# Kernel tuning notes

Hardware: AMD Instinct MI355X
Metric: run time of the kernel (lower is better)

Reference implementation:

```python
import jax, jax.numpy as jnp
import numpy as np

PATCH = 16
CH = 3


def setup_inputs() -> dict:
    key = jax.random.key(0)
    k1, k2, k3 = jax.random.split(key, 3)
    B, H = 16, 512
    embed_dim = PATCH * PATCH * CH  # 768
    x = jax.random.normal(k1, (B, CH, H, H), dtype=jnp.float32)
    fan_in = CH * PATCH * PATCH
    w = jax.random.normal(k2, (embed_dim, CH, PATCH, PATCH), dtype=jnp.float32) / np.float32(np.sqrt(fan_in))
    b = jax.random.normal(k3, (embed_dim,), dtype=jnp.float32) * 0.01
    return {"x": x, "w": w, "b": b}


def reference(x, w, b):
    p = w.shape[2]                      # patch_size
    B, C, imgsize, _ = x.shape
    pn = imgsize // p                   # patch_num (NOTE: pre-padding count, as in source)
    # zero-pad by one patch on every side
    xp = jnp.pad(x, ((0, 0), (0, 0), (p, p), (p, p)))
    # strided patch-embed conv: [B, embed_dim, pn+2, pn+2]
    xt = jax.lax.conv_general_dilated(xp, w, window_strides=(p, p), padding='VALID')
    xt = xt + b[None, :, None, None]
    B1, C1, H1, W1 = xt.shape           # H1 = W1 = pn + 2
    xt = xt.reshape(B1, C1, H1 * W1)
    # same (buggy-looking but faithful) index set / stride-pn neighbors as the source
    idxs = jnp.array([i * pn + j for i in range(1, pn - 1) for j in range(1, pn)], dtype=jnp.int32)
    inv8 = jnp.float32(1.0 / 8.0)

    def body(buf, idx):
        # torch aliases x_final=x_temp, so reads see earlier in-place writes -> sequential scan
        s = (buf[:, :, idx - pn] + buf[:, :, idx + pn]
             + buf[:, :, idx - 1] + buf[:, :, idx + 1]
             + buf[:, :, idx - pn - 1] + buf[:, :, idx - pn + 1]
             + buf[:, :, idx + pn - 1] + buf[:, :, idx + pn + 1]) * inv8
        return buf.at[:, :, idx].set(s), None

    xf, _ = jax.lax.scan(body, xt, idxs)
    side = imgsize + 2 * p              # embed_dim*H1*W1 == C*side*side by construction
    out = xf.reshape(B1, C, side, side)
    return out[:, :, p:imgsize + p, p:imgsize + p]
```

## Files before the change

kernel.cpp:

```cpp
#include <hip/hip_runtime.h>
#include <hip/hip_bf16.h>


typedef __attribute__((ext_vector_type(8))) short s8v;
typedef __attribute__((ext_vector_type(4))) float f4v;
typedef __attribute__((ext_vector_type(8))) unsigned short us8;
typedef __attribute__((ext_vector_type(4))) unsigned short us4;

__device__ __forceinline__ unsigned short f2bf(float f) {
    __hip_bfloat16 h = __float2bfloat16(f);
    return *reinterpret_cast<unsigned short*>(&h);
}
__device__ __forceinline__ float bf2f(unsigned short u) {
    union { unsigned int i; float f; } c; c.i = (unsigned int)u << 16; return c.f;
}

__global__ __launch_bounds__(256) void prep_w_k(const float* __restrict__ w,
                                                unsigned short* __restrict__ w_bf) {
    int g = blockIdx.x * 256 + threadIdx.x;
    int f = g << 3;
    const float4 v0 = *(const float4*)(w + f);
    const float4 v1 = *(const float4*)(w + f + 4);
    us8 u;
    u[0] = f2bf(v0.x); u[1] = f2bf(v0.y); u[2] = f2bf(v0.z); u[3] = f2bf(v0.w);
    u[4] = f2bf(v1.x); u[5] = f2bf(v1.y); u[6] = f2bf(v1.z); u[7] = f2bf(v1.w);
    *(us8*)(w_bf + f) = u;
}

__global__ __launch_bounds__(512, 4) void conv_gemm_rs_k(const float* __restrict__ x,
                                                         const unsigned short* __restrict__ W,
                                                         const float* __restrict__ bias,
                                                         unsigned short* __restrict__ xt) {
    __shared__ __align__(16) unsigned short As[2][128 * 32];
    __shared__ __align__(16) unsigned short Bs[2][192 * 32];
    const int tid  = threadIdx.x;
    const int lane = tid & 63, wv = tid >> 6;
    const int wr = wv >> 2, wc = wv & 3;
    const int m0 = blockIdx.x << 7;
    const int n0 = blockIdx.y * 192;
    const int bb = m0 >> 10;
    const int ph0 = (m0 >> 5) & 31;

    const int arow = tid >> 2, ach = tid & 3;
    const int phl  = arow >> 5, pw = arow & 31;
    const int aoff = (arow << 5) + ((ach ^ ((arow >> 1) & 3)) << 3);
    const float* xbase = x + (size_t)bb * 786432 + (ph0 + phl) * 8192
                           + (ach >> 1) * 512 + (pw << 4) + ((ach & 1) << 3);

    const int brow = tid >> 1, bpair = tid & 1;
    const int bxr  = (brow >> 1) & 3;
    const int boff0 = (brow << 5) + ((((bpair << 1))     ^ bxr) << 3);
    const int boff1 = (brow << 5) + ((((bpair << 1) | 1) ^ bxr) << 3);
    const unsigned short* wbase = W + (size_t)(n0 + brow) * 768 + (bpair << 4);

    float4 xr_[2][2];
    us8    wf_[2][2];

    auto gload = [&](int s, int t) {
        const float* sp = xbase + (t >> 3) * 262144 + (t & 7) * 1024;
        xr_[s][0] = *(const float4*)(sp);
        xr_[s][1] = *(const float4*)(sp + 4);
        if (tid < 384) {
            const unsigned short* ws = wbase + (t << 5);
            wf_[s][0] = *(const us8*)(ws);
            wf_[s][1] = *(const us8*)(ws + 8);
        }
    };
    auto store = [&](int s, int buf) {
        us8 lo;
        lo[0]=f2bf(xr_[s][0].x); lo[1]=f2bf(xr_[s][0].y);
        lo[2]=f2bf(xr_[s][0].z); lo[3]=f2bf(xr_[s][0].w);
        lo[4]=f2bf(xr_[s][1].x); lo[5]=f2bf(xr_[s][1].y);
        lo[6]=f2bf(xr_[s][1].z); lo[7]=f2bf(xr_[s][1].w);
        *(us8*)(As[buf] + aoff) = lo;
        if (tid < 384) {
            *(us8*)(Bs[buf] + boff0) = wf_[s][0];
            *(us8*)(Bs[buf] + boff1) = wf_[s][1];
        }
    };

    f4v acc[4][3] = {};
    gload(0, 0);
    store(0, 0);
    __syncthreads();

    const int cq = lane >> 4, l15 = lane & 15;
    #pragma unroll
    for (int t = 0; t < 24; ++t) {
        const int p = t & 1;
        if (t < 23) gload(p ^ 1, t + 1);
        s8v a[4], b[3];
        #pragma unroll
        for (int mi = 0; mi < 4; ++mi) {
            int ra = (wr << 6) + (mi << 4) + l15;
            a[mi] = *(const s8v*)(As[p] + (ra << 5) + ((cq ^ ((ra >> 1) & 3)) << 3));
        }
        #pragma unroll
        for (int ni = 0; ni < 3; ++ni) {
            int rb = wc * 48 + (ni << 4) + l15;
            b[ni] = *(const s8v*)(Bs[p] + (rb << 5) + ((cq ^ ((rb >> 1) & 3)) << 3));
        }
        #pragma unroll
        for (int mi = 0; mi < 4; ++mi)
            #pragma unroll
            for (int ni = 0; ni < 3; ++ni)
                acc[mi][ni] = __builtin_amdgcn_mfma_f32_16x16x32_bf16(a[mi], b[ni], acc[mi][ni], 0, 0, 0);
        if (t < 23) store(p ^ 1, p ^ 1);
        __syncthreads();
    }

    #pragma unroll
    for (int mi = 0; mi < 4; ++mi) {
        int m  = m0 + (wr << 6) + (mi << 4) + (cq << 2);
        int ph = (m >> 5) & 31, pwm = m & 31;
        unsigned short* dst = xt + (((size_t)bb * 768) << 10) + (ph << 5) + pwm;
        #pragma unroll
        for (int ni = 0; ni < 3; ++ni) {
            int n = n0 + wc * 48 + (ni << 4) + l15;
            float bv = bias[n];
            us4 o;
            o[0] = f2bf(acc[mi][ni][0] + bv);
            o[1] = f2bf(acc[mi][ni][1] + bv);
            o[2] = f2bf(acc[mi][ni][2] + bv);
            o[3] = f2bf(acc[mi][ni][3] + bv);
            *(us4*)(dst + ((size_t)n << 10)) = o;
        }
    }
}

__global__ __launch_bounds__(256) void scan_emit_k(const unsigned short* __restrict__ xt,
                                                   const float* __restrict__ bias,
                                                   float* __restrict__ out) {
    const int grp = (blockIdx.x * 256 + threadIdx.x) >> 5;
    const int j   = threadIdx.x & 31;
    const int b   = grp / 768;
    const int c1  = grp - b * 768;
    const unsigned short* basep = xt + ((size_t)grp << 10);
    const float bias_c = bias[c1];
    float* baseo = out + (size_t)b * 786432 + (size_t)(c1 >> 8) * 262144;

    int rem = (c1 & 255) * 1156 + j;
    int ey  = rem / 544;
    int ex  = rem - ey * 544;
    int eo  = (ey - 16) * 512 + (ex - 16);

    auto estep = [&](float v) {
        if (((unsigned)(ex - 16) < 512u) & ((unsigned)(ey - 16) < 512u))
            baseo[eo] = v;
        ex += 32;
        int wrp = (ex >= 544);
        ex -= wrp ? 544 : 0;
        ey += wrp;
        eo += wrp ? 0 : 32;
    };
    auto sel = [&](int p) -> float {
        unsigned int h = (unsigned int)p / 34u;
        unsigned int w = (unsigned int)p - h * 34u;
        if ((h == 0u) | (h == 33u) | (w == 0u) | (w == 33u)) return bias_c;
        return bf2f(basep[(h - 1u) * 32u + (w - 1u)]);
    };

    float co = sel( 32 + j);
    float no = sel( 64 + j);
    float o2 = sel( 96 + j);
    float o3 = sel(128 + j);
    estep(bias_c);
    float pn   = bias_c;
    float po_h = bias_c;
    float h_co = __shfl(co, 0, 32);
    float h_no = __shfl(no, 0, 32);
    float h_o2 = __shfl(o2, 0, 32);
    float rr   = __shfl_down(co, 1, 32);
    if (j == 31) rr = h_no;

    for (int i = 1; i <= 30; ++i) {
        float ld = sel((i + 4) * 32 + j);
        float UL = __shfl_up(pn, 1, 32);   if (j == 1)  UL = po_h;
        float UR = __shfl_down(pn, 1, 32); if (j == 31) UR = h_co;
        float D1 = __shfl_up(no, 1, 32);
        float D3 = __shfl_down(no, 1, 32); if (j == 31) D3 = h_o2;
        float bv = (((UL + pn) + (UR + rr)) + ((D1 + no) + D3)) * 0.125f;
        if (j == 1) bv += h_co * 0.125f;
        float t;
        t = __shfl_up(bv, 1, 32);  bv += (j > 1) ? 0.125f * t : 0.f;
        t = __shfl_up(bv, 2, 32);  bv += (j > 2) ? 0.015625f * t : 0.f;
        t = __shfl_up(bv, 4, 32);  bv += (j > 4) ? 2.44140625e-4f * t : 0.f;
        estep((j == 0) ? co : bv);
        rr   = D3;
        pn   = bv;
        po_h = h_co; h_co = h_no; h_no = h_o2;
        h_o2 = __shfl(o3, 0, 32);
        co = no; no = o2; o2 = o3; o3 = ld;
    }
    estep(co);
    estep(no);
    estep(o2);
    estep(o3);
    estep(sel(1120 + j));
    if (j < 4) estep(bias_c);
}

extern "C" void kernel_launch(void* const* d_in, const int* in_sizes, int n_in,
                              void* d_out, int out_size, void* d_ws, size_t ws_size,
                              hipStream_t stream) {
    const float* x    = (const float*)d_in[0];
    const float* w    = (const float*)d_in[1];
    const float* bias = (const float*)d_in[2];
    float* out = (float*)d_out;
    unsigned short* xt = (unsigned short*)d_ws;

    unsigned short* w_bf = (unsigned short*)d_out;

    prep_w_k<<<288, 256, 0, stream>>>(w, w_bf);
    conv_gemm_rs_k<<<dim3(128, 4), 512, 0, stream>>>(x, w_bf, bias, xt);
    scan_emit_k<<<1536, 256, 0, stream>>>(xt, bias, out);
}
```

Baseline: 67.94 us.

## Pre-im2col input to bf16 and stage GEMM tiles via direct global-to-LDS loads

```diff
diff --git a/kernel.cpp b/kernel.cpp
--- a/kernel.cpp
+++ b/kernel.cpp
@@ -15,98 +15,98 @@
     union { unsigned int i; float f; } c; c.i = (unsigned int)u << 16; return c.f;
 }
 
-__global__ __launch_bounds__(256) void prep_w_k(const float* __restrict__ w,
-                                                unsigned short* __restrict__ w_bf) {
-    int g = blockIdx.x * 256 + threadIdx.x;
-    int f = g << 3;
-    const float4 v0 = *(const float4*)(w + f);
-    const float4 v1 = *(const float4*)(w + f + 4);
-    us8 u;
-    u[0] = f2bf(v0.x); u[1] = f2bf(v0.y); u[2] = f2bf(v0.z); u[3] = f2bf(v0.w);
-    u[4] = f2bf(v1.x); u[5] = f2bf(v1.y); u[6] = f2bf(v1.z); u[7] = f2bf(v1.w);
-    *(us8*)(w_bf + f) = u;
-}
-
-__global__ __launch_bounds__(512, 4) void conv_gemm_rs_k(const float* __restrict__ x,
-                                                         const unsigned short* __restrict__ W,
-                                                         const float* __restrict__ bias,
-                                                         unsigned short* __restrict__ xt) {
+__device__ __forceinline__ void gload_lds16(const void* g, void* l) {
+    __builtin_amdgcn_global_load_lds(
+        (const __attribute__((address_space(1))) unsigned int*)g,
+        (__attribute__((address_space(3))) unsigned int*)l,
+        16, 0, 0);
+}
+
+__global__ __launch_bounds__(256) void prep_k(const float* __restrict__ x,
+                                              const float* __restrict__ w,
+                                              unsigned short* __restrict__ a_bf,
+                                              unsigned short* __restrict__ w_bf) {
+    const int bid = blockIdx.x;
+    if (bid < 6144) {
+        int g = bid * 256 + threadIdx.x;
+        int f = g << 3;
+        int wc = f & 511;
+        int h  = (f >> 9) & 511;
+        int cb = f >> 18;
+        int c  = cb % 3, b = cb / 3;
+        const float4 v0 = *(const float4*)(x + f);
+        const float4 v1 = *(const float4*)(x + f + 4);
+        int m = (b << 10) + ((h >> 4) << 5) + (wc >> 4);
+        int k = (c << 8) + ((h & 15) << 4) + (wc & 15);
+        us8 o;
+        o[0] = f2bf(v0.x); o[1] = f2bf(v0.y); o[2] = f2bf(v0.z); o[3] = f2bf(v0.w);
+        o[4] = f2bf(v1.x); o[5] = f2bf(v1.y); o[6] = f2bf(v1.z); o[7] = f2bf(v1.w);
+        *(us8*)(a_bf + (size_t)m * 768 + k) = o;
+    } else {
+        int g = (bid - 6144) * 256 + threadIdx.x;
+        int f = g << 3;
+        const float4 v0 = *(const float4*)(w + f);
+        const float4 v1 = *(const float4*)(w + f + 4);
+        us8 u;
+        u[0] = f2bf(v0.x); u[1] = f2bf(v0.y); u[2] = f2bf(v0.z); u[3] = f2bf(v0.w);
+        u[4] = f2bf(v1.x); u[5] = f2bf(v1.y); u[6] = f2bf(v1.z); u[7] = f2bf(v1.w);
+        *(us8*)(w_bf + f) = u;
+    }
+}
+
+__global__ __launch_bounds__(256) void conv_gemm_k(const unsigned short* __restrict__ A,
+                                                   const unsigned short* __restrict__ W,
+                                                   const float* __restrict__ bias,
+                                                   unsigned short* __restrict__ xt) {
     __shared__ __align__(16) unsigned short As[2][128 * 32];
-    __shared__ __align__(16) unsigned short Bs[2][192 * 32];
+    __shared__ __align__(16) unsigned short Bs[2][128 * 32];
     const int tid  = threadIdx.x;
     const int lane = tid & 63, wv = tid >> 6;
-    const int wr = wv >> 2, wc = wv & 3;
-    const int m0 = blockIdx.x << 7;
-    const int n0 = blockIdx.y * 192;
+    const int wr = wv >> 1, wc = wv & 1;
+    const int m0 = blockIdx.x << 7, n0 = blockIdx.y << 7;
     const int bb = m0 >> 10;
-    const int ph0 = (m0 >> 5) & 31;
-
-    const int arow = tid >> 2, ach = tid & 3;
-    const int phl  = arow >> 5, pw = arow & 31;
-    const int aoff = (arow << 5) + ((ach ^ ((arow >> 1) & 3)) << 3);
-    const float* xbase = x + (size_t)bb * 786432 + (ph0 + phl) * 8192
-                           + (ach >> 1) * 512 + (pw << 4) + ((ach & 1) << 3);
-
-    const int brow = tid >> 1, bpair = tid & 1;
-    const int bxr  = (brow >> 1) & 3;
-    const int boff0 = (brow << 5) + ((((bpair << 1))     ^ bxr) << 3);
-    const int boff1 = (brow << 5) + ((((bpair << 1) | 1) ^ bxr) << 3);
-    const unsigned short* wbase = W + (size_t)(n0 + brow) * 768 + (bpair << 4);
-
-    float4 xr_[2][2];
-    us8    wf_[2][2];
-
-    auto gload = [&](int s, int t) {
-        const float* sp = xbase + (t >> 3) * 262144 + (t & 7) * 1024;
-        xr_[s][0] = *(const float4*)(sp);
-        xr_[s][1] = *(const float4*)(sp + 4);
-        if (tid < 384) {
-            const unsigned short* ws = wbase + (t << 5);
-            wf_[s][0] = *(const us8*)(ws);
-            wf_[s][1] = *(const us8*)(ws + 8);
-        }
+
+    f4v acc[4][4] = {};
+
+    const int l2 = lane >> 2;
+    const int kx = ((lane & 3) ^ ((l2 >> 1) & 3)) << 3;
+    const unsigned short* gA = A + (size_t)(m0 + (wv << 5) + l2) * 768 + kx;
+    const unsigned short* gB = W + (size_t)(n0 + (wv << 5) + l2) * 768 + kx;
+
+    auto stage = [&](int buf, int k0) {
+        gload_lds16(gA + k0,            As[buf] + (wv << 10));
+        gload_lds16(gA + k0 + 16 * 768, As[buf] + (wv << 10) + 512);
+        gload_lds16(gB + k0,            Bs[buf] + (wv << 10));
+        gload_lds16(gB + k0 + 16 * 768, Bs[buf] + (wv << 10) + 512);
     };
-    auto store = [&](int s, int buf) {
-        us8 lo;
-        lo[0]=f2bf(xr_[s][0].x); lo[1]=f2bf(xr_[s][0].y);
-        lo[2]=f2bf(xr_[s][0].z); lo[3]=f2bf(xr_[s][0].w);
-        lo[4]=f2bf(xr_[s][1].x); lo[5]=f2bf(xr_[s][1].y);
-        lo[6]=f2bf(xr_[s][1].z); lo[7]=f2bf(xr_[s][1].w);
-        *(us8*)(As[buf] + aoff) = lo;
-        if (tid < 384) {
-            *(us8*)(Bs[buf] + boff0) = wf_[s][0];
-            *(us8*)(Bs[buf] + boff1) = wf_[s][1];
-        }
-    };
-
-    f4v acc[4][3] = {};
-    gload(0, 0);
-    store(0, 0);
+
+    stage(0, 0);
+    asm volatile("s_waitcnt vmcnt(0)" ::: "memory");
     __syncthreads();
 
     const int cq = lane >> 4, l15 = lane & 15;
-    #pragma unroll
+    int cur = 0;
     for (int t = 0; t < 24; ++t) {
-        const int p = t & 1;
-        if (t < 23) gload(p ^ 1, t + 1);
-        s8v a[4], b[3];
+        if (t < 23) stage(cur ^ 1, (t + 1) << 5);
+        s8v a[4], b[4];
         #pragma unroll
         for (int mi = 0; mi < 4; ++mi) {
             int ra = (wr << 6) + (mi << 4) + l15;
-            a[mi] = *(const s8v*)(As[p] + (ra << 5) + ((cq ^ ((ra >> 1) & 3)) << 3));
+            a[mi] = *(const s8v*)(As[cur] + (ra << 5) + ((cq ^ ((ra >> 1) & 3)) << 3));
         }
         #pragma unroll
-        for (int ni = 0; ni < 3; ++ni) {
-            int rb = wc * 48 + (ni << 4) + l15;
-            b[ni] = *(const s8v*)(Bs[p] + (rb << 5) + ((cq ^ ((rb >> 1) & 3)) << 3));
+        for (int ni = 0; ni < 4; ++ni) {
+            int rb = (wc << 6) + (ni << 4) + l15;
+            b[ni] = *(const s8v*)(Bs[cur] + (rb << 5) + ((cq ^ ((rb >> 1) & 3)) << 3));
         }
         #pragma unroll
         for (int mi = 0; mi < 4; ++mi)
             #pragma unroll
-            for (int ni = 0; ni < 3; ++ni)
+            for (int ni = 0; ni < 4; ++ni)
                 acc[mi][ni] = __builtin_amdgcn_mfma_f32_16x16x32_bf16(a[mi], b[ni], acc[mi][ni], 0, 0, 0);
-        if (t < 23) store(p ^ 1, p ^ 1);
+        asm volatile("s_waitcnt vmcnt(0)" ::: "memory");
         __syncthreads();
+        cur ^= 1;
     }
 
     #pragma unroll
@@ -115,8 +115,8 @@
         int ph = (m >> 5) & 31, pwm = m & 31;
         unsigned short* dst = xt + (((size_t)bb * 768) << 10) + (ph << 5) + pwm;
         #pragma unroll
-        for (int ni = 0; ni < 3; ++ni) {
-            int n = n0 + wc * 48 + (ni << 4) + l15;
+        for (int ni = 0; ni < 4; ++ni) {
+            int n = n0 + (wc << 6) + (ni << 4) + l15;
             float bv = bias[n];
             us4 o;
             o[0] = f2bf(acc[mi][ni][0] + bv);
@@ -209,9 +209,10 @@
     float* out = (float*)d_out;
     unsigned short* xt = (unsigned short*)d_ws;
 
-    unsigned short* w_bf = (unsigned short*)d_out;
-
-    prep_w_k<<<288, 256, 0, stream>>>(w, w_bf);
-    conv_gemm_rs_k<<<dim3(128, 4), 512, 0, stream>>>(x, w_bf, bias, xt);
+    unsigned short* a_bf = (unsigned short*)d_out;
+    unsigned short* w_bf = a_bf + (size_t)16384 * 768;
+
+    prep_k<<<6432, 256, 0, stream>>>(x, w, a_bf, w_bf);
+    conv_gemm_k<<<dim3(128, 6), 256, 0, stream>>>(a_bf, w_bf, bias, xt);
     scan_emit_k<<<1536, 256, 0, stream>>>(xt, bias, out);
 }
```

New measurement: 78.68 us. 1.16x slower.
